# Performance work log

Hardware: AMD Instinct MI355X
Metric: run time of the kernel (lower is better)

## Reference

```python
import jax, jax.numpy as jnp
import numpy as np

L = 43          # number of classes
C = L + 3       # <eps>, 'O', 'I-', + L class symbols
B = 128
T = 4096
NEG = jnp.float32(-1e30)


def setup_inputs() -> dict:
    key = jax.random.key(0)
    k1, k2, k3, k4 = jax.random.split(key, 4)
    logits = jax.random.normal(k1, (B, T, C), dtype=jnp.float32)
    log_probs = jax.nn.log_softmax(logits, axis=-1)
    input_lens = jax.random.randint(k2, (B,), T // 2, T + 1).astype(jnp.int32)
    labels = jax.random.randint(k3, (B, T), 1, C).astype(jnp.int32)  # valid (non-eps) symbols
    # den_scores parameter: one raw score per denominator arc (2L+4 arcs).
    # Layout: [0]=0->0 'O', [1:L+1]=0->0 labels, [L+1]=0->1 'I-', [L+2]=0->final,
    #         [L+3]=1->1 'I-', [L+4:2L+4]=1->0 labels.
    den_params = 0.01 * jax.random.normal(k4, (2 * L + 4,), dtype=jnp.float32)
    return {"log_probs": log_probs, "den_params": den_params,
            "input_lens": input_lens, "labels": labels}


def reference(log_probs, den_params, input_lens, labels):
    Bb, Tt, Cc = log_probs.shape
    Ll = Cc - 3
    # set_scores_stochastic_: per-source-state log-softmax of arc scores
    g0 = jax.nn.log_softmax(den_params[: Ll + 3])   # state-0 outgoing arcs
    g1 = jax.nn.log_softmax(den_params[Ll + 3:])    # state-1 outgoing arcs
    s_O, s0_lab, s_0I, s_fin = g0[0], g0[1:Ll + 1], g0[Ll + 1], g0[Ll + 2]
    s_1I, s1_lab = g1[0], g1[1:]

    mask = jnp.arange(Tt)[None, :] < input_lens[:, None]          # [B,T]

    # ---- numerator: linear FSA intersected with emissions = path score ----
    tok_lp = jnp.take_along_axis(log_probs, labels[..., None], axis=-1)[..., 0]
    num = jnp.sum(jnp.where(mask, tok_lp, 0.0), axis=1)           # [B]

    # ---- denominator: log-semiring forward DP over the 2-state topology ----
    lp_t = jnp.moveaxis(log_probs, 1, 0)    # [T,B,C]
    mask_t = jnp.moveaxis(mask, 1, 0)       # [T,B]

    def step(alpha, inputs):
        lp, m = inputs                       # lp [B,C], m [B]
        a0, a1 = alpha[:, 0], alpha[:, 1]
        lp_lab = lp[:, 3:]                   # emissions for class symbols, [B,L]
        # into state 0: 0->0 on 'O', 0->0 on each label, 1->0 on each label
        terms0 = jnp.concatenate([
            (a0 + s_O + lp[:, 1])[:, None],
            a0[:, None] + s0_lab[None, :] + lp_lab,
            a1[:, None] + s1_lab[None, :] + lp_lab,
        ], axis=1)
        n0 = jax.scipy.special.logsumexp(terms0, axis=1)
        # into state 1: 0->1 and 1->1, both on 'I-'
        terms1 = jnp.stack([a0 + s_0I + lp[:, 2], a1 + s_1I + lp[:, 2]], axis=1)
        n1 = jax.scipy.special.logsumexp(terms1, axis=1)
        new = jnp.stack([n0, n1], axis=1)
        new = jnp.where(m[:, None], new, alpha)  # frozen past each seq's length
        return new, None

    alpha0 = jnp.concatenate(
        [jnp.zeros((Bb, 1), log_probs.dtype), jnp.full((Bb, 1), NEG, log_probs.dtype)], axis=1)
    alpha, _ = jax.lax.scan(step, alpha0, (lp_t, mask_t))
    den = alpha[:, 0] + s_fin                                    # final arc 0->2 on -1

    return jnp.sum(num - den)
```

## Files before the change

kernel.cpp:

```cpp
#include <hip/hip_runtime.h>

#define BB 128
#define TT 4096
#define LL 43
#define CC 46
#define CHUNK 256
#define NC (TT / CHUNK)
#define TPB 256
#define NEGF (-1e30f)
#define L2E 1.44269504088896340736f
#define LN2 0.69314718055994530942f

__device__ __forceinline__ float la2(float x, float y) {
    float mx = fmaxf(x, y), mn = fminf(x, y);
    return mx + log2f(1.0f + exp2f(mn - mx));
}

__global__ __launch_bounds__(TPB) void crf_chunk(
    const float* __restrict__ lp, const float* __restrict__ dp,
    const int* __restrict__ lens, const int* __restrict__ labels,
    float* __restrict__ res) {
    __shared__ float tile[CHUNK * CC];
    __shared__ float2 pp[LL];
    __shared__ float sc[4];
    __shared__ float wres[TPB / 64][5];

    int b = blockIdx.y, c = blockIdx.x;
    int t0 = c * CHUNK;
    int len = lens[b];
    int tid = threadIdx.x;
    float* r = res + (b * NC + c) * 8;

    if (t0 >= len) {
        if (tid == 0) { r[0] = 0.f; r[1] = NEGF; r[2] = NEGF; r[3] = 0.f; r[4] = 0.f; }
        return;
    }

    {
        int wv = tid >> 6, ln = tid & 63;
        const float* gsrc = lp + (size_t)(b * TT + t0) * CC;
        for (int s = wv; s < CC; s += TPB / 64) {
            const float* g = gsrc + s * 256 + ln * 4;
            float* l = tile + s * 256;
            __builtin_amdgcn_global_load_lds(
                (const __attribute__((address_space(1))) void*)g,
                (__attribute__((address_space(3))) void*)l, 16, 0, 0);
        }
    }

    if (tid < 64) {
        int lane = tid;
        float x0 = (lane < CC) ? dp[lane] : NEGF;
        float x1 = (lane < LL + 1) ? dp[CC + lane] : NEGF;
        float mx0 = x0, mx1 = x1;
        #pragma unroll
        for (int m = 1; m < 64; m <<= 1) {
            mx0 = fmaxf(mx0, __shfl_xor(mx0, m));
            mx1 = fmaxf(mx1, __shfl_xor(mx1, m));
        }
        float e0 = (lane < CC) ? expf(x0 - mx0) : 0.0f;
        float e1 = (lane < LL + 1) ? expf(x1 - mx1) : 0.0f;
        float s0 = e0, s1 = e1;
        #pragma unroll
        for (int m = 1; m < 64; m <<= 1) {
            s0 += __shfl_xor(s0, m);
            s1 += __shfl_xor(s1, m);
        }
        float g0 = x0 - mx0 - logf(s0);
        float g1 = x1 - mx1 - logf(s1);
        if (lane >= 1 && lane <= LL) { pp[lane - 1].x = expf(g0); pp[lane - 1].y = expf(g1); }
        if (lane == 0) { sc[0] = expf(g0); sc[2] = g1 * L2E; }
        if (lane == LL + 1) sc[1] = g0 * L2E;
        if (lane == LL + 2) sc[3] = g0 * L2E;
    }

    int t = t0 + tid;
    int lab = labels[b * TT + t];
    __syncthreads();

    const float* vr = tile + tid * CC;
    float m00, m01, m10, m11, tok;
    {
        const float2* vr2 = (const float2*)vr;
        float2 c01 = vr2[0];
        float2 c23 = vr2[1];
        float w1 = exp2f(L2E * c01.y);
        float v2s = L2E * c23.x;
        float dot0 = sc[0] * w1;
        float dot1 = 0.f;
        {
            float w = exp2f(L2E * c23.y);
            float2 p = pp[0];
            dot0 = fmaf(p.x, w, dot0);
            dot1 = fmaf(p.y, w, dot1);
        }
        #pragma unroll
        for (int k = 2; k <= 22; ++k) {
            float2 v = vr2[k];
            float wa = exp2f(L2E * v.x), wb = exp2f(L2E * v.y);
            float2 pa = pp[2 * k - 3], pb = pp[2 * k - 2];
            dot0 = fmaf(pa.x, wa, dot0); dot1 = fmaf(pa.y, wa, dot1);
            dot0 = fmaf(pb.x, wb, dot0); dot1 = fmaf(pb.y, wb, dot1);
        }
        m00 = log2f(dot0);
        m01 = log2f(dot1);
        m10 = sc[1] + v2s;
        m11 = sc[2] + v2s;
        tok = vr[lab];
    }
    if (t >= len) { m00 = 0.f; m01 = NEGF; m10 = NEGF; m11 = 0.f; tok = 0.f; }

    int lane = tid & 63;
    #pragma unroll
    for (int m = 1; m < 64; m <<= 1) {
        float p00 = __shfl_xor(m00, m), p01 = __shfl_xor(m01, m);
        float p10 = __shfl_xor(m10, m), p11 = __shfl_xor(m11, m);
        bool up = (lane & m) != 0;
        float a00 = up ? m00 : p00, a01 = up ? m01 : p01;
        float a10 = up ? m10 : p10, a11 = up ? m11 : p11;
        float b00 = up ? p00 : m00, b01 = up ? p01 : m01;
        float b10 = up ? p10 : m10, b11 = up ? p11 : m11;
        m00 = la2(a00 + b00, a01 + b10);
        m01 = la2(a00 + b01, a01 + b11);
        m10 = la2(a10 + b00, a11 + b10);
        m11 = la2(a10 + b01, a11 + b11);
        tok += __shfl_xor(tok, m);
    }
    if (lane == 0) {
        int w = tid >> 6;
        wres[w][0] = m00; wres[w][1] = m01; wres[w][2] = m10; wres[w][3] = m11; wres[w][4] = tok;
    }
    __syncthreads();

    if (tid == 0) {
        float c00 = wres[0][0], c01 = wres[0][1], c10 = wres[0][2], c11 = wres[0][3];
        float num = wres[0][4];
        #pragma unroll
        for (int w = 1; w < TPB / 64; ++w) {
            float a00 = wres[w][0], a01 = wres[w][1], a10 = wres[w][2], a11 = wres[w][3];
            float n00 = la2(a00 + c00, a01 + c10);
            float n01 = la2(a00 + c01, a01 + c11);
            float n10 = la2(a10 + c00, a11 + c10);
            float n11 = la2(a10 + c01, a11 + c11);
            c00 = n00; c01 = n01; c10 = n10; c11 = n11;
            num += wres[w][4];
        }
        r[0] = c00; r[1] = c01; r[2] = c10; r[3] = c11; r[4] = num;
    }
}

__global__ void crf_final(const float* __restrict__ dp, const float* __restrict__ res,
                          float* __restrict__ out) {
    __shared__ float sfin2sh;
    __shared__ float part[2];
    int tid = threadIdx.x;
    if (tid < 64) {
        float x0 = (tid < CC) ? dp[tid] : NEGF;
        float mx0 = x0;
        #pragma unroll
        for (int m = 1; m < 64; m <<= 1) mx0 = fmaxf(mx0, __shfl_xor(mx0, m));
        float e0 = (tid < CC) ? expf(x0 - mx0) : 0.0f;
        float s0 = e0;
        #pragma unroll
        for (int m = 1; m < 64; m <<= 1) s0 += __shfl_xor(s0, m);
        if (tid == LL + 2) sfin2sh = (x0 - mx0 - logf(s0)) * L2E;
    }
    __syncthreads();
    float a0 = 0.f, a1 = NEGF, num = 0.f;
    #pragma unroll 4
    for (int c = 0; c < NC; ++c) {
        const float* r = res + (tid * NC + c) * 8;
        float n0 = la2(r[0] + a0, r[1] + a1);
        float n1 = la2(r[2] + a0, r[3] + a1);
        a0 = n0; a1 = n1; num += r[4];
    }
    float val = num - (a0 + sfin2sh) * LN2;
    #pragma unroll
    for (int m = 1; m < 64; m <<= 1) val += __shfl_xor(val, m);
    if ((tid & 63) == 0) part[tid >> 6] = val;
    __syncthreads();
    if (tid == 0) out[0] = part[0] + part[1];
}

extern "C" void kernel_launch(void* const* d_in, const int* in_sizes, int n_in,
                              void* d_out, int out_size, void* d_ws, size_t ws_size,
                              hipStream_t stream) {
    const float* lp = (const float*)d_in[0];
    const float* dp = (const float*)d_in[1];
    const int* lens = (const int*)d_in[2];
    const int* labels = (const int*)d_in[3];
    float* out = (float*)d_out;
    float* res = (float*)d_ws;

    hipLaunchKernelGGL(crf_chunk, dim3(NC, BB), dim3(TPB), 0, stream,
                       lp, dp, lens, labels, res);
    hipLaunchKernelGGL(crf_final, dim3(1), dim3(128), 0, stream, dp, res, out);
}
```

Baseline: 154.6 us.

## Read log-prob rows directly from global memory, drop LDS tile staging

Removes the global_load_lds staging of the 256x46 chunk into shared memory. Each thread now reads its own row straight from global memory, with uncoalesced per-thread row strides. Every wave computes its own copy of the arc-score softmax, which removes the __syncthreads before the main compute and cuts LDS use so that more blocks can be resident (launch bounds set to 4). The trade is strided global loads and the softmax being recomputed four times per block.

Measured after the change: 169.0 us. 9.3% more time.

```diff
diff --git a/kernel.cpp b/kernel.cpp
--- a/kernel.cpp
+++ b/kernel.cpp
@@ -7,6 +7,7 @@
 #define CHUNK 256
 #define NC (TT / CHUNK)
 #define TPB 256
+#define NW (TPB / 64)
 #define NEGF (-1e30f)
 #define L2E 1.44269504088896340736f
 #define LN2 0.69314718055994530942f
@@ -16,19 +17,19 @@
     return mx + log2f(1.0f + exp2f(mn - mx));
 }
 
-__global__ __launch_bounds__(TPB) void crf_chunk(
+__global__ __launch_bounds__(TPB, 4) void crf_chunk(
     const float* __restrict__ lp, const float* __restrict__ dp,
     const int* __restrict__ lens, const int* __restrict__ labels,
     float* __restrict__ res) {
-    __shared__ float tile[CHUNK * CC];
-    __shared__ float2 pp[LL];
-    __shared__ float sc[4];
-    __shared__ float wres[TPB / 64][5];
+    __shared__ float2 pp[NW][LL + 1];
+    __shared__ float sc[NW][4];
+    __shared__ float wres[NW][5];
 
     int b = blockIdx.y, c = blockIdx.x;
     int t0 = c * CHUNK;
     int len = lens[b];
     int tid = threadIdx.x;
+    int wv = tid >> 6, lane = tid & 63;
     float* r = res + (b * NC + c) * 8;
 
     if (t0 >= len) {
@@ -37,19 +38,6 @@
     }
 
     {
-        int wv = tid >> 6, ln = tid & 63;
-        const float* gsrc = lp + (size_t)(b * TT + t0) * CC;
-        for (int s = wv; s < CC; s += TPB / 64) {
-            const float* g = gsrc + s * 256 + ln * 4;
-            float* l = tile + s * 256;
-            __builtin_amdgcn_global_load_lds(
-                (const __attribute__((address_space(1))) void*)g,
-                (__attribute__((address_space(3))) void*)l, 16, 0, 0);
-        }
-    }
-
-    if (tid < 64) {
-        int lane = tid;
         float x0 = (lane < CC) ? dp[lane] : NEGF;
         float x1 = (lane < LL + 1) ? dp[CC + lane] : NEGF;
         float mx0 = x0, mx1 = x1;
@@ -68,29 +56,28 @@
         }
         float g0 = x0 - mx0 - logf(s0);
         float g1 = x1 - mx1 - logf(s1);
-        if (lane >= 1 && lane <= LL) { pp[lane - 1].x = expf(g0); pp[lane - 1].y = expf(g1); }
-        if (lane == 0) { sc[0] = expf(g0); sc[2] = g1 * L2E; }
-        if (lane == LL + 1) sc[1] = g0 * L2E;
-        if (lane == LL + 2) sc[3] = g0 * L2E;
+        if (lane >= 1 && lane <= LL) { pp[wv][lane - 1].x = expf(g0); pp[wv][lane - 1].y = expf(g1); }
+        if (lane == 0) { sc[wv][0] = expf(g0); sc[wv][2] = g1 * L2E; }
+        if (lane == LL + 1) sc[wv][1] = g0 * L2E;
+        if (lane == LL + 2) sc[wv][3] = g0 * L2E;
     }
 
     int t = t0 + tid;
+    const float* row = lp + (size_t)(b * TT + t) * CC;
     int lab = labels[b * TT + t];
-    __syncthreads();
-
-    const float* vr = tile + tid * CC;
     float m00, m01, m10, m11, tok;
     {
-        const float2* vr2 = (const float2*)vr;
+        const float2* vr2 = (const float2*)row;
         float2 c01 = vr2[0];
         float2 c23 = vr2[1];
+        tok = row[lab];
         float w1 = exp2f(L2E * c01.y);
         float v2s = L2E * c23.x;
-        float dot0 = sc[0] * w1;
+        float dot0 = sc[wv][0] * w1;
         float dot1 = 0.f;
         {
             float w = exp2f(L2E * c23.y);
-            float2 p = pp[0];
+            float2 p = pp[wv][0];
             dot0 = fmaf(p.x, w, dot0);
             dot1 = fmaf(p.y, w, dot1);
         }
@@ -98,19 +85,17 @@
         for (int k = 2; k <= 22; ++k) {
             float2 v = vr2[k];
             float wa = exp2f(L2E * v.x), wb = exp2f(L2E * v.y);
-            float2 pa = pp[2 * k - 3], pb = pp[2 * k - 2];
+            float2 pa = pp[wv][2 * k - 3], pb = pp[wv][2 * k - 2];
             dot0 = fmaf(pa.x, wa, dot0); dot1 = fmaf(pa.y, wa, dot1);
             dot0 = fmaf(pb.x, wb, dot0); dot1 = fmaf(pb.y, wb, dot1);
         }
         m00 = log2f(dot0);
         m01 = log2f(dot1);
-        m10 = sc[1] + v2s;
-        m11 = sc[2] + v2s;
-        tok = vr[lab];
+        m10 = sc[wv][1] + v2s;
+        m11 = sc[wv][2] + v2s;
     }
     if (t >= len) { m00 = 0.f; m01 = NEGF; m10 = NEGF; m11 = 0.f; tok = 0.f; }
 
-    int lane = tid & 63;
     #pragma unroll
     for (int m = 1; m < 64; m <<= 1) {
         float p00 = __shfl_xor(m00, m), p01 = __shfl_xor(m01, m);
@@ -127,8 +112,7 @@
         tok += __shfl_xor(tok, m);
     }
     if (lane == 0) {
-        int w = tid >> 6;
-        wres[w][0] = m00; wres[w][1] = m01; wres[w][2] = m10; wres[w][3] = m11; wres[w][4] = tok;
+        wres[wv][0] = m00; wres[wv][1] = m01; wres[wv][2] = m10; wres[wv][3] = m11; wres[wv][4] = tok;
     }
     __syncthreads();
 
@@ -136,7 +120,7 @@
         float c00 = wres[0][0], c01 = wres[0][1], c10 = wres[0][2], c11 = wres[0][3];
         float num = wres[0][4];
         #pragma unroll
-        for (int w = 1; w < TPB / 64; ++w) {
+        for (int w = 1; w < NW; ++w) {
             float a00 = wres[w][0], a01 = wres[w][1], a10 = wres[w][2], a11 = wres[w][3];
             float n00 = la2(a00 + c00, a01 + c10);
             float n01 = la2(a00 + c01, a01 + c11);
```

## Shrink chunk to one wavefront per block and drop cross-wave combine

Applied to the files above, without the earlier changes.

Each block now handles a 64-step chunk with a single 64-lane wavefront instead of 256 steps over four wavefronts. This removes the shared-memory cross-wave matrix combine and its second barrier, and lets more blocks share each CU with a smaller LDS tile. The cost is four times as many chunk results, so the single-block final kernel now does a serial loop over 64 chunks per sequence instead of 16, which may dominate.

New measurement: 157.6 us. Within noise of the previous version (+1.9%).

```diff
diff --git a/kernel.cpp b/kernel.cpp
--- a/kernel.cpp
+++ b/kernel.cpp
@@ -4,9 +4,8 @@
 #define TT 4096
 #define LL 43
 #define CC 46
-#define CHUNK 256
+#define CHUNK 64
 #define NC (TT / CHUNK)
-#define TPB 256
 #define NEGF (-1e30f)
 #define L2E 1.44269504088896340736f
 #define LN2 0.69314718055994530942f
@@ -16,40 +15,45 @@
     return mx + log2f(1.0f + exp2f(mn - mx));
 }
 
-__global__ __launch_bounds__(TPB) void crf_chunk(
+__global__ __launch_bounds__(64) void crf_chunk(
     const float* __restrict__ lp, const float* __restrict__ dp,
     const int* __restrict__ lens, const int* __restrict__ labels,
     float* __restrict__ res) {
     __shared__ float tile[CHUNK * CC];
-    __shared__ float2 pp[LL];
+    __shared__ float2 pp[LL + 1];
     __shared__ float sc[4];
-    __shared__ float wres[TPB / 64][5];
 
     int b = blockIdx.y, c = blockIdx.x;
     int t0 = c * CHUNK;
     int len = lens[b];
-    int tid = threadIdx.x;
+    int lane = threadIdx.x;
     float* r = res + (b * NC + c) * 8;
 
     if (t0 >= len) {
-        if (tid == 0) { r[0] = 0.f; r[1] = NEGF; r[2] = NEGF; r[3] = 0.f; r[4] = 0.f; }
+        if (lane == 0) { r[0] = 0.f; r[1] = NEGF; r[2] = NEGF; r[3] = 0.f; r[4] = 0.f; }
         return;
     }
 
     {
-        int wv = tid >> 6, ln = tid & 63;
         const float* gsrc = lp + (size_t)(b * TT + t0) * CC;
-        for (int s = wv; s < CC; s += TPB / 64) {
-            const float* g = gsrc + s * 256 + ln * 4;
+        #pragma unroll
+        for (int s = 0; s < 11; ++s) {
+            const float* g = gsrc + s * 256 + lane * 4;
             float* l = tile + s * 256;
+            __builtin_amdgcn_global_load_lds(
+                (const __attribute__((address_space(1))) void*)g,
+                (__attribute__((address_space(3))) void*)l, 16, 0, 0);
+        }
+        if (lane < 32) {
+            const float* g = gsrc + 11 * 256 + lane * 4;
+            float* l = tile + 11 * 256;
             __builtin_amdgcn_global_load_lds(
                 (const __attribute__((address_space(1))) void*)g,
                 (__attribute__((address_space(3))) void*)l, 16, 0, 0);
         }
     }
 
-    if (tid < 64) {
-        int lane = tid;
+    {
         float x0 = (lane < CC) ? dp[lane] : NEGF;
         float x1 = (lane < LL + 1) ? dp[CC + lane] : NEGF;
         float mx0 = x0, mx1 = x1;
@@ -74,16 +78,17 @@
         if (lane == LL + 2) sc[3] = g0 * L2E;
     }
 
-    int t = t0 + tid;
+    int t = t0 + lane;
     int lab = labels[b * TT + t];
     __syncthreads();
 
-    const float* vr = tile + tid * CC;
+    const float* vr = tile + lane * CC;
     float m00, m01, m10, m11, tok;
     {
         const float2* vr2 = (const float2*)vr;
         float2 c01 = vr2[0];
         float2 c23 = vr2[1];
+        tok = vr[lab];
         float w1 = exp2f(L2E * c01.y);
         float v2s = L2E * c23.x;
         float dot0 = sc[0] * w1;
@@ -106,11 +111,9 @@
         m01 = log2f(dot1);
         m10 = sc[1] + v2s;
         m11 = sc[2] + v2s;
-        tok = vr[lab];
     }
     if (t >= len) { m00 = 0.f; m01 = NEGF; m10 = NEGF; m11 = 0.f; tok = 0.f; }
 
-    int lane = tid & 63;
     #pragma unroll
     for (int m = 1; m < 64; m <<= 1) {
         float p00 = __shfl_xor(m00, m), p01 = __shfl_xor(m01, m);
@@ -127,25 +130,7 @@
         tok += __shfl_xor(tok, m);
     }
     if (lane == 0) {
-        int w = tid >> 6;
-        wres[w][0] = m00; wres[w][1] = m01; wres[w][2] = m10; wres[w][3] = m11; wres[w][4] = tok;
-    }
-    __syncthreads();
-
-    if (tid == 0) {
-        float c00 = wres[0][0], c01 = wres[0][1], c10 = wres[0][2], c11 = wres[0][3];
-        float num = wres[0][4];
-        #pragma unroll
-        for (int w = 1; w < TPB / 64; ++w) {
-            float a00 = wres[w][0], a01 = wres[w][1], a10 = wres[w][2], a11 = wres[w][3];
-            float n00 = la2(a00 + c00, a01 + c10);
-            float n01 = la2(a00 + c01, a01 + c11);
-            float n10 = la2(a10 + c00, a11 + c10);
-            float n11 = la2(a10 + c01, a11 + c11);
-            c00 = n00; c01 = n01; c10 = n10; c11 = n11;
-            num += wres[w][4];
-        }
-        r[0] = c00; r[1] = c01; r[2] = c10; r[3] = c11; r[4] = num;
+        r[0] = m00; r[1] = m01; r[2] = m10; r[3] = m11; r[4] = tok;
     }
 }
 
@@ -192,7 +177,7 @@
     float* out = (float*)d_out;
     float* res = (float*)d_ws;
 
-    hipLaunchKernelGGL(crf_chunk, dim3(NC, BB), dim3(TPB), 0, stream,
+    hipLaunchKernelGGL(crf_chunk, dim3(NC, BB), dim3(64), 0, stream,
                        lp, dp, lens, labels, res);
     hipLaunchKernelGGL(crf_final, dim3(1), dim3(128), 0, stream, dp, res, out);
 }
```
